# Kernel tuning notes

Measured on AMD Instinct MI355X. Metric: run time of the kernel, lower is better.

## Reference

```python
import jax, jax.numpy as jnp
import numpy as np

N = 100000      # nodes (categories_nums[0])
E = 1600000     # edges
FEAT = 16       # features_num
HID = 32        # hidden
IDE = 16        # id_embed_size
EMB = 8         # embed_size
CAT_MAX = 1000  # categorical vocab (categories_nums[1:])
K = 3           # TAGConv hops (sparse=False)
NC = 2          # num_class
IN_DIM = IDE + 2 * EMB + HID  # 64 -> TAGConv input
EPS = 1e-5


def layer_norm(x, g, b):
    m = jnp.mean(x, axis=-1, keepdims=True)
    v = jnp.mean((x - m) ** 2, axis=-1, keepdims=True)
    return (x - m) * jax.lax.rsqrt(v + EPS) * g + b


def setup_inputs() -> dict:
    key = jax.random.key(0)
    ks = jax.random.split(key, 20)
    s = 0.05
    return {
        "x": jax.random.normal(ks[0], (N, FEAT), jnp.float32),
        "edge_index": jax.random.randint(ks[1], (2, E), 0, N, jnp.int64),
        "edge_weight": jax.random.uniform(ks[2], (E,), jnp.float32),
        "categories_value": jax.random.randint(ks[3], (N, 3), 0, CAT_MAX, jnp.int64),
        "id_table": jax.random.normal(ks[4], (N, IDE), jnp.float32) * s,
        "lin0_id_W": jax.random.normal(ks[5], (IDE, IDE), jnp.float32) * s,
        "lin0_id_b": jnp.zeros((IDE,), jnp.float32),
        "emb1": jax.random.normal(ks[6], (CAT_MAX, EMB), jnp.float32) * s,
        "emb2": jax.random.normal(ks[7], (CAT_MAX, EMB), jnp.float32) * s,
        "lin0_emb_W": jax.random.normal(ks[8], (2 * EMB, 2 * EMB), jnp.float32) * s,
        "lin0_emb_b": jnp.zeros((2 * EMB,), jnp.float32),
        "lin0_W": jax.random.normal(ks[9], (FEAT, HID), jnp.float32) * s,
        "lin0_b": jnp.zeros((HID,), jnp.float32),
        "ln0_g": jnp.ones((IN_DIM,), jnp.float32),
        "ln0_b": jnp.zeros((IN_DIM,), jnp.float32),
        "tag_W": jax.random.normal(ks[10], (K + 1, IN_DIM, HID), jnp.float32) * s,
        "tag_b": jnp.zeros((HID,), jnp.float32),
        "ln1_g": jnp.ones((HID,), jnp.float32),
        "ln1_b": jnp.zeros((HID,), jnp.float32),
        "lin1_W": jax.random.normal(ks[11], (HID, NC), jnp.float32) * s,
        "lin1_b": jnp.zeros((NC,), jnp.float32),
    }


def reference(x, edge_index, edge_weight, categories_value, id_table, lin0_id_W,
              lin0_id_b, emb1, emb2, lin0_emb_W, lin0_emb_b, lin0_W, lin0_b,
              ln0_g, ln0_b, tag_W, tag_b, ln1_g, ln1_b, lin1_W, lin1_b):
    # eval mode: dropouts are identity
    h = jax.nn.elu(x @ lin0_W + lin0_b)                       # [N, HID]
    ide = id_table[categories_value[:, 0]]                    # [N, IDE]
    ide = jax.nn.elu(ide @ lin0_id_W + lin0_id_b)
    er = jnp.concatenate([emb1[categories_value[:, 1]],
                          emb2[categories_value[:, 2]]], axis=1)  # [N, 2*EMB]
    er = jax.nn.elu(er @ lin0_emb_W + lin0_emb_b)
    feat = jnp.concatenate([ide, h, er], axis=1)              # [N, IN_DIM]
    feat = layer_norm(feat, ln0_g, ln0_b)

    # TAGConv: gcn_norm without self-loops, K-hop propagation
    row, col = edge_index[0], edge_index[1]                   # source -> target
    deg = jax.ops.segment_sum(edge_weight, col, num_segments=N)
    dis = jnp.where(deg > 0, deg ** -0.5, 0.0)
    norm = dis[row] * edge_weight * dis[col]                  # [E]

    out = feat @ tag_W[0]                                     # [N, HID]
    xk = feat
    for k in range(1, K + 1):
        xk = jax.ops.segment_sum(xk[row] * norm[:, None], col, num_segments=N)
        out = out + xk @ tag_W[k]
    out = out + tag_b

    out = jax.nn.relu(out)
    out = layer_norm(out, ln1_g, ln1_b)
    out = out @ lin1_W + lin1_b                               # [N, NC]
    return jax.nn.log_softmax(out, axis=-1)
```

## Files before the change

### kernel.cpp

```cpp
#include <hip/hip_runtime.h>
#include <hip/hip_bf16.h>

typedef unsigned short u16;
typedef unsigned int   u32;
typedef unsigned long long u64;
typedef u32 u32x2 __attribute__((ext_vector_type(2)));
typedef u32 u32x4 __attribute__((ext_vector_type(4)));

#define FIX_SCALE 16777216.0f
#define FIX_INV   (1.0f / 16777216.0f)
#define CNT_SHIFT 40
#define DEG_MASK  ((1ULL << CNT_SHIFT) - 1)

__device__ __forceinline__ float b2f(u16 u) { return __uint_as_float(((u32)u) << 16); }
__device__ __forceinline__ u16 f2b(float f) {
    u32 u = __float_as_uint(f);
    return (u16)((u + 0x7FFFu + ((u >> 16) & 1u)) >> 16);
}
__device__ __forceinline__ float elu(float v) { return v > 0.f ? v : expm1f(v); }
__device__ __forceinline__ float ldf(const void* p, size_t i, int f32) {
    return f32 ? ((const float*)p)[i] : b2f(((const u16*)p)[i]);
}
__device__ __forceinline__ float plo(u32 a) { return __uint_as_float(a << 16); }
__device__ __forceinline__ float phi(u32 a) { return __uint_as_float(a & 0xFFFF0000u); }

__global__ void k_flags(const u32* __restrict__ gw, const int* __restrict__ ei,
                        const int* __restrict__ cat, int* __restrict__ flags) {
    if (threadIdx.x == 0 && blockIdx.x == 0) {
        flags[0] = (gw[0] == 0x3F800000u) ? 1 : 0;
        flags[1] = ((ei[1]  | ei[3]  | ei[5]  | ei[7])  == 0) ? 2 : 1;
        flags[2] = ((cat[1] | cat[3] | cat[5] | cat[7]) == 0) ? 2 : 1;
    }
}

__global__ __launch_bounds__(256) void k_feathist(
    const void* __restrict__ x, const int* __restrict__ cat,
    const void* __restrict__ id_table, const void* __restrict__ W_id, const void* __restrict__ b_id,
    const void* __restrict__ emb1, const void* __restrict__ emb2,
    const void* __restrict__ W_emb, const void* __restrict__ b_emb,
    const void* __restrict__ W0, const void* __restrict__ b0,
    const void* __restrict__ g0, const void* __restrict__ bb0,
    u32* __restrict__ feat,
    const int* __restrict__ ei, const void* __restrict__ ew,
    u64* __restrict__ packed, u16* __restrict__ rank,
    const int* __restrict__ flags, int N, int E, int nbN)
{
    __shared__ float sW0[512];
    __shared__ float sb0[32];
    __shared__ float sWid[256];
    __shared__ float sbid[16];
    __shared__ float sWe[256];
    __shared__ float sbe[16];
    __shared__ float sg[64], sb[64];
    int tid = threadIdx.x;
    int f32 = flags[0], s = flags[1], cs = flags[2];

    int e0 = blockIdx.x * 512 + tid;
    int e1 = e0 + 256;
    u64 old0 = 0, old1 = 0;
    bool h0 = (e0 < E), h1 = (e1 < E);
    const int* colp = ei + (size_t)E * s;
    if (h0) {
        int cdst = colp[(size_t)e0 * s];
        float w = ldf(ew, e0, f32);
        old0 = atomicAdd(&packed[cdst], (1ULL << CNT_SHIFT) | (u64)(w * FIX_SCALE + 0.5f));
    }
    if (h1) {
        int cdst = colp[(size_t)e1 * s];
        float w = ldf(ew, e1, f32);
        old1 = atomicAdd(&packed[cdst], (1ULL << CNT_SHIFT) | (u64)(w * FIX_SCALE + 0.5f));
    }

    if (blockIdx.x < nbN) {
        for (int i = tid; i < 512; i += 256) sW0[i] = ldf(W0, i, f32);
        if (tid < 32) sb0[tid] = ldf(b0, tid, f32);
        sWid[tid] = ldf(W_id, tid, f32);
        if (tid < 16) sbid[tid] = ldf(b_id, tid, f32);
        sWe[tid] = ldf(W_emb, tid, f32);
        if (tid < 16) sbe[tid] = ldf(b_emb, tid, f32);
        if (tid < 64) { sg[tid] = ldf(g0, tid, f32); sb[tid] = ldf(bb0, tid, f32); }
        __syncthreads();

        int i = blockIdx.x * 256 + tid;
        if (i < N) {
            size_t cb = (size_t)i * 3 * cs;
            int c0 = cat[cb], c1 = cat[cb + cs], c2 = cat[cb + 2 * cs];
            float f[64];
            {
                float t[16];
                #pragma unroll
                for (int q = 0; q < 16; q++) t[q] = ldf(id_table, (size_t)c0 * 16 + q, f32);
                #pragma unroll
                for (int j = 0; j < 16; j++) {
                    float a = sbid[j];
                    #pragma unroll
                    for (int ff = 0; ff < 16; ff++) a += t[ff] * sWid[ff * 16 + j];
                    f[j] = elu(a);
                }
            }
            {
                float t[16];
                #pragma unroll
                for (int q = 0; q < 16; q++) t[q] = ldf(x, (size_t)i * 16 + q, f32);
                #pragma unroll
                for (int j = 0; j < 32; j++) {
                    float a = sb0[j];
                    #pragma unroll
                    for (int ff = 0; ff < 16; ff++) a += t[ff] * sW0[ff * 32 + j];
                    f[16 + j] = elu(a);
                }
            }
            {
                float t[16];
                #pragma unroll
                for (int q = 0; q < 8; q++) t[q] = ldf(emb1, (size_t)c1 * 8 + q, f32);
                #pragma unroll
                for (int q = 0; q < 8; q++) t[8 + q] = ldf(emb2, (size_t)c2 * 8 + q, f32);
                #pragma unroll
                for (int j = 0; j < 16; j++) {
                    float a = sbe[j];
                    #pragma unroll
                    for (int ff = 0; ff < 16; ff++) a += t[ff] * sWe[ff * 16 + j];
                    f[48 + j] = elu(a);
                }
            }
            float m = 0.f;
            #pragma unroll
            for (int d = 0; d < 64; d++) m += f[d];
            m *= (1.f / 64.f);
            float var = 0.f;
            #pragma unroll
            for (int d = 0; d < 64; d++) { float df = f[d] - m; var += df * df; }
            var *= (1.f / 64.f);
            float rs = rsqrtf(var + 1e-5f);
            #pragma unroll
            for (int d = 0; d < 64; d++) f[d] = (f[d] - m) * rs * sg[d] + sb[d];

            u32* fp = feat + (size_t)i * 32;
            #pragma unroll
            for (int q = 0; q < 32; q++) fp[q] = ((u32)f2b(f[2 * q + 1]) << 16) | f2b(f[2 * q]);
        }
    }
    if (h0) rank[e0] = (u16)(old0 >> CNT_SHIFT);
    if (h1) rank[e1] = (u16)(old1 >> CNT_SHIFT);
}

__global__ __launch_bounds__(256) void k_zproj(
    const u32* __restrict__ feat, const void* __restrict__ tagW,
    float* __restrict__ oacc, u32* __restrict__ z1, u32* __restrict__ z2, u32* __restrict__ z3,
    const int* __restrict__ flags, int N)
{
    __shared__ u32x4 sF[512];
    int tid = threadIdx.x;
    int f32 = flags[0];
    int wid = tid >> 6;
    int lane = tid & 63;
    int j = lane & 31;
    int dh = lane >> 5;

    float w[32];
    {
        size_t base = (size_t)wid * 2048 + (size_t)dh * 1024 + j;
        #pragma unroll
        for (int dd = 0; dd < 32; dd++) w[dd] = ldf(tagW, base + (size_t)dd * 32, f32);
    }

    int nb0 = blockIdx.x * 64;
    int nv = N - nb0; if (nv > 64) nv = 64; if (nv < 0) nv = 0;
    for (int i = tid; i < nv * 8; i += 256)
        sF[i] = ((const u32x4*)feat)[(size_t)nb0 * 8 + i];
    __syncthreads();

    u32* zp = (wid == 1) ? z1 : (wid == 2) ? z2 : z3;

    #pragma unroll 2
    for (int n = 0; n < nv; n++) {
        const u32x4* fp = sF + n * 8 + dh * 4;
        u32x4 r0 = fp[0], r1 = fp[1], r2 = fp[2], r3 = fp[3];
        float za = 0.f, zb = 0.f;
        za += plo(r0.x) * w[0];  zb += phi(r0.x) * w[1];
        za += plo(r0.y) * w[2];  zb += phi(r0.y) * w[3];
        za += plo(r0.z) * w[4];  zb += phi(r0.z) * w[5];
        za += plo(r0.w) * w[6];  zb += phi(r0.w) * w[7];
        za += plo(r1.x) * w[8];  zb += phi(r1.x) * w[9];
        za += plo(r1.y) * w[10]; zb += phi(r1.y) * w[11];
        za += plo(r1.z) * w[12]; zb += phi(r1.z) * w[13];
        za += plo(r1.w) * w[14]; zb += phi(r1.w) * w[15];
        za += plo(r2.x) * w[16]; zb += phi(r2.x) * w[17];
        za += plo(r2.y) * w[18]; zb += phi(r2.y) * w[19];
        za += plo(r2.z) * w[20]; zb += phi(r2.z) * w[21];
        za += plo(r2.w) * w[22]; zb += phi(r2.w) * w[23];
        za += plo(r3.x) * w[24]; zb += phi(r3.x) * w[25];
        za += plo(r3.y) * w[26]; zb += phi(r3.y) * w[27];
        za += plo(r3.z) * w[28]; zb += phi(r3.z) * w[29];
        za += plo(r3.w) * w[30]; zb += phi(r3.w) * w[31];
        float z = za + zb;
        z += __shfl_xor(z, 32);

        int gnode = nb0 + n;
        if (wid == 0) {
            if (lane < 32) oacc[(size_t)gnode * 32 + j] = z;
        } else {
            float zlo = __shfl(z, 2 * lane);
            float zhi = __shfl(z, 2 * lane + 1);
            if (lane < 16)
                zp[(size_t)gnode * 16 + lane] = ((u32)f2b(zhi) << 16) | f2b(zlo);
        }
    }
}

__global__ __launch_bounds__(256) void k_scan1(const u64* __restrict__ packed, int* __restrict__ ebuf,
                                               int* __restrict__ bsum, float* __restrict__ dis, int N)
{
    __shared__ int sdat[256];
    int tid = threadIdx.x;
    int i = blockIdx.x * 256 + tid;
    u64 pv = (i < N) ? packed[i] : 0ULL;
    int v = (int)(pv >> CNT_SHIFT);
    sdat[tid] = v;
    __syncthreads();
    for (int off = 1; off < 256; off <<= 1) {
        int t = (tid >= off) ? sdat[tid - off] : 0;
        __syncthreads();
        sdat[tid] += t;
        __syncthreads();
    }
    if (i < N) {
        ebuf[i] = sdat[tid] - v;
        u64 db = pv & DEG_MASK;
        dis[i] = db ? rsqrtf((float)db * FIX_INV) : 0.f;
    }
    if (tid == 255) bsum[blockIdx.x] = sdat[255];
}

__global__ __launch_bounds__(512) void k_scan2(const int* __restrict__ bsum, int* __restrict__ boff, int NB)
{
    __shared__ int sdat[512];
    __shared__ int scarry;
    int tid = threadIdx.x;
    if (tid == 0) scarry = 0;
    __syncthreads();
    for (int base = 0; base < NB; base += 512) {
        int i = base + tid;
        int v = (i < NB) ? bsum[i] : 0;
        sdat[tid] = v;
        __syncthreads();
        for (int off = 1; off < 512; off <<= 1) {
            int t = (tid >= off) ? sdat[tid - off] : 0;
            __syncthreads();
            sdat[tid] += t;
            __syncthreads();
        }
        if (i < NB) boff[i] = scarry + sdat[tid] - v;
        __syncthreads();
        if (tid == 0) scarry += sdat[511];
        __syncthreads();
    }
}

__global__ __launch_bounds__(256) void k_scan3(const int* __restrict__ ebuf, const int* __restrict__ boff,
                                               int* __restrict__ rowptr, int N, int E)
{
    int i = blockIdx.x * 256 + threadIdx.x;
    if (i >= N) return;
    rowptr[i] = boff[blockIdx.x] + ebuf[i];
    if (i == N - 1) rowptr[N] = E;
}

__global__ __launch_bounds__(256) void k_scatter(const int* __restrict__ ei, const void* __restrict__ ew,
                                                 const float* __restrict__ dis, const u16* __restrict__ rank,
                                                 const int* __restrict__ rowptr, int2* __restrict__ csr,
                                                 const int* __restrict__ flags, int E)
{
    int f32 = flags[0], s = flags[1];
    const int* row = ei;
    const int* col = ei + (size_t)E * s;
    int e = blockIdx.x * 256 + threadIdx.x;
    if (e >= E) return;
    int r = row[(size_t)e * s], c = col[(size_t)e * s];
    float nrm = dis[r] * ldf(ew, e, f32) * dis[c];
    csr[rowptr[c] + (int)rank[e]] = make_int2(r, __float_as_int(nrm));
}

template<int ADD>
__global__ __launch_bounds__(256) void k_ahop(
    const u32* __restrict__ zin, const u32* __restrict__ zadd, u32* __restrict__ uout,
    const int* __restrict__ rowptr, const int2* __restrict__ csr, int N)
{
    int tid = threadIdx.x;
    int node = blockIdx.x * 4 + (tid >> 6);
    if (node >= N) return;
    int lane = tid & 63;
    int o = (lane >> 3) & 7;
    int c = lane & 7;
    int start = rowptr[node], end = rowptr[node + 1];

    const u32x2* fin2 = (const u32x2*)zin;
    float v0 = 0.f, v1 = 0.f, v2 = 0.f, v3 = 0.f;
    int e = start;
    for (; e + 16 <= end; e += 16) {
        int2 ma = csr[e + o];
        int2 mb = csr[e + 8 + o];
        u32x2 aa = fin2[(size_t)(u32)ma.x * 8 + c];
        u32x2 ab = fin2[(size_t)(u32)mb.x * 8 + c];
        float wa = __int_as_float(ma.y), wb = __int_as_float(mb.y);
        v0 += plo(aa.x) * wa; v1 += phi(aa.x) * wa; v2 += plo(aa.y) * wa; v3 += phi(aa.y) * wa;
        v0 += plo(ab.x) * wb; v1 += phi(ab.x) * wb; v2 += plo(ab.y) * wb; v3 += phi(ab.y) * wb;
    }
    for (; e < end; e += 8) {
        int ee = e + o;
        int2 m = (ee < end) ? csr[ee] : make_int2(0, 0);
        u32x2 a = fin2[(size_t)(u32)m.x * 8 + c];
        float w = __int_as_float(m.y);
        v0 += plo(a.x) * w; v1 += phi(a.x) * w; v2 += plo(a.y) * w; v3 += phi(a.y) * w;
    }
    v0 += __shfl_xor(v0, 8);  v1 += __shfl_xor(v1, 8);  v2 += __shfl_xor(v2, 8);  v3 += __shfl_xor(v3, 8);
    v0 += __shfl_xor(v0, 16); v1 += __shfl_xor(v1, 16); v2 += __shfl_xor(v2, 16); v3 += __shfl_xor(v3, 16);
    v0 += __shfl_xor(v0, 32); v1 += __shfl_xor(v1, 32); v2 += __shfl_xor(v2, 32); v3 += __shfl_xor(v3, 32);

    if (lane < 8) {
        if (ADD) {
            u32x2 z = ((const u32x2*)zadd)[(size_t)node * 8 + lane];
            v0 += plo(z.x); v1 += phi(z.x); v2 += plo(z.y); v3 += phi(z.y);
        }
        u32x2 pw;
        pw.x = ((u32)f2b(v1) << 16) | f2b(v0);
        pw.y = ((u32)f2b(v3) << 16) | f2b(v2);
        ((u32x2*)uout)[(size_t)node * 8 + lane] = pw;
    }
}

__global__ __launch_bounds__(256) void k_head(
    const float* __restrict__ oacc, const u32* __restrict__ t1,
    const void* __restrict__ tag_b,
    const void* __restrict__ g1, const void* __restrict__ b1,
    const void* __restrict__ W1, const void* __restrict__ bb1,
    void* __restrict__ out, const int* __restrict__ flags, int N)
{
    __shared__ float stb[32], sg[32], sbb[32], sW1[64], sb1v[2];
    int tid = threadIdx.x;
    int f32 = flags[0];
    if (tid < 32) { stb[tid] = ldf(tag_b, tid, f32); sg[tid] = ldf(g1, tid, f32); sbb[tid] = ldf(b1, tid, f32); }
    if (tid < 64) sW1[tid] = ldf(W1, tid, f32);
    if (tid < 2) sb1v[tid] = ldf(bb1, tid, f32);
    __syncthreads();

    int i = blockIdx.x * 256 + tid;
    if (i >= N) return;

    float acc[32];
    const float4* oa4 = (const float4*)(oacc + (size_t)i * 32);
    #pragma unroll
    for (int q = 0; q < 8; q++) {
        float4 t = oa4[q];
        acc[4 * q] = t.x; acc[4 * q + 1] = t.y; acc[4 * q + 2] = t.z; acc[4 * q + 3] = t.w;
    }
    const u32x2* tp = (const u32x2*)t1 + (size_t)i * 8;
    #pragma unroll
    for (int q = 0; q < 8; q++) {
        u32x2 z = tp[q];
        acc[4 * q]     += plo(z.x); acc[4 * q + 1] += phi(z.x);
        acc[4 * q + 2] += plo(z.y); acc[4 * q + 3] += phi(z.y);
    }
    float o[32]; float m = 0.f;
    #pragma unroll
    for (int j = 0; j < 32; j++) { float t = acc[j] + stb[j]; t = t > 0.f ? t : 0.f; o[j] = t; m += t; }
    m *= (1.f / 32.f);
    float var = 0.f;
    #pragma unroll
    for (int j = 0; j < 32; j++) { float d = o[j] - m; var += d * d; }
    var *= (1.f / 32.f);
    float rs = rsqrtf(var + 1e-5f);
    float z0 = sb1v[0], z1 = sb1v[1];
    #pragma unroll
    for (int j = 0; j < 32; j++) {
        float t = (o[j] - m) * rs * sg[j] + sbb[j];
        z0 += t * sW1[2 * j];
        z1 += t * sW1[2 * j + 1];
    }
    float mx = fmaxf(z0, z1);
    float l = mx + logf(expf(z0 - mx) + expf(z1 - mx));
    if (f32) {
        ((float*)out)[(size_t)i * 2]     = z0 - l;
        ((float*)out)[(size_t)i * 2 + 1] = z1 - l;
    } else {
        *((u32*)((u16*)out + (size_t)i * 2)) = ((u32)f2b(z1 - l) << 16) | f2b(z0 - l);
    }
}

extern "C" void kernel_launch(void* const* d_in, const int* in_sizes, int n_in,
                              void* d_out, int out_size, void* d_ws, size_t ws_size,
                              hipStream_t stream)
{
    const void* x        = d_in[0];
    const int*  ei       = (const int*)d_in[1];
    const void* ew       = d_in[2];
    const int*  cat      = (const int*)d_in[3];
    const void* id_table = d_in[4];
    const void* W_id     = d_in[5];
    const void* b_id     = d_in[6];
    const void* emb1     = d_in[7];
    const void* emb2     = d_in[8];
    const void* W_emb    = d_in[9];
    const void* b_emb    = d_in[10];
    const void* W0       = d_in[11];
    const void* b0       = d_in[12];
    const void* g0       = d_in[13];
    const void* bb0      = d_in[14];
    const void* tagW     = d_in[15];
    const void* tag_b    = d_in[16];
    const void* g1       = d_in[17];
    const void* b1       = d_in[18];
    const void* W1       = d_in[19];
    const void* bb1      = d_in[20];

    int N = in_sizes[0] / 16;
    int E = in_sizes[2];
    int nb = (N + 255) / 256;
    int eb = (E + 255) / 256;
    int eb2 = (E + 511) / 512;
    int zb = (N + 63) / 64;

    char* ws = (char*)d_ws;
    size_t off = 0;
    int*   flags  = (int*)(ws + off);   off += 256;
    float* oacc   = (float*)(ws + off); off += (size_t)N * 32 * 4;
    u32*   feat   = (u32*)(ws + off);   off += (size_t)N * 32 * 4;
    u32*   z1     = (u32*)(ws + off);   off += (size_t)N * 16 * 4;
    u32*   z2     = (u32*)(ws + off);   off += (size_t)N * 16 * 4;
    u32*   z3     = (u32*)(ws + off);   off += (size_t)N * 16 * 4;
    u32*   u2     = (u32*)(ws + off);   off += (size_t)N * 16 * 4;
    int2*  csr    = (int2*)(ws + off);  off += (size_t)E * 8;
    int*   rowptr = (int*)(ws + off);   off += ((size_t)N + 1) * 4;
    off = (off + 255) & ~(size_t)255;
    u16*   rank   = (u16*)(ws + off);   off += (size_t)E * 2;
    off = (off + 255) & ~(size_t)255;
    u64*   packed = (u64*)(ws + off);   off += (size_t)N * 8;
    int*   ebuf   = (int*)(ws + off);   off += (size_t)N * 4;
    float* dis    = (float*)(ws + off); off += (size_t)N * 4;
    int*   bsum   = (int*)(ws + off);   off += (size_t)nb * 4;
    int*   boff   = (int*)(ws + off);   off += (size_t)nb * 4;

    hipMemsetAsync(packed, 0, (size_t)N * 8, stream);
    k_flags<<<1, 64, 0, stream>>>((const u32*)g0, ei, cat, flags);

    k_feathist<<<eb2, 256, 0, stream>>>(x, cat, id_table, W_id, b_id, emb1, emb2, W_emb, b_emb,
                                        W0, b0, g0, bb0, feat,
                                        ei, ew, packed, rank, flags, N, E, nb);
    k_zproj<<<zb, 256, 0, stream>>>(feat, tagW, oacc, z1, z2, z3, flags, N);

    k_scan1<<<nb, 256, 0, stream>>>(packed, ebuf, bsum, dis, N);
    k_scan2<<<1, 512, 0, stream>>>(bsum, boff, nb);
    k_scan3<<<nb, 256, 0, stream>>>(ebuf, boff, rowptr, N, E);
    k_scatter<<<eb, 256, 0, stream>>>(ei, ew, dis, rank, rowptr, csr, flags, E);

    int hb = (N + 3) / 4;
    k_ahop<1><<<hb, 256, 0, stream>>>(z3, z2, u2, rowptr, csr, N);
    k_ahop<1><<<hb, 256, 0, stream>>>(u2, z1, z3, rowptr, csr, N);
    k_ahop<0><<<hb, 256, 0, stream>>>(z3, z1, z2, rowptr, csr, N);
    k_head<<<nb, 256, 0, stream>>>(oacc, z2, tag_b, g1, b1, W1, bb1, d_out, flags, N);
}
```

Before: 386.4 us.

## Fuse output head into final hop and merge block-scan kernels

The final propagation hop now runs the bias, ReLU, LayerNorm, linear layer and log-softmax itself, using 8-lane shuffles across the per-node lanes. This removes the separate head kernel and the write and re-read of the last hop result. The second and third scan kernels are also merged into one: each block recomputes its offset by summing all preceding block sums. That drops a single-block launch but adds redundant reads of the block sums, which grow with the block index.

```diff
diff --git a/kernel.cpp b/kernel.cpp
--- a/kernel.cpp
+++ b/kernel.cpp
@@ -233,37 +233,23 @@
     if (tid == 255) bsum[blockIdx.x] = sdat[255];
 }
 
-__global__ __launch_bounds__(512) void k_scan2(const int* __restrict__ bsum, int* __restrict__ boff, int NB)
-{
-    __shared__ int sdat[512];
-    __shared__ int scarry;
+__global__ __launch_bounds__(256) void k_scanX(const int* __restrict__ bsum, const int* __restrict__ ebuf,
+                                               int* __restrict__ rowptr, int N, int E)
+{
+    __shared__ int sred[256];
+    int b = blockIdx.x;
     int tid = threadIdx.x;
-    if (tid == 0) scarry = 0;
+    int acc = 0;
+    for (int i = tid; i < b; i += 256) acc += bsum[i];
+    sred[tid] = acc;
     __syncthreads();
-    for (int base = 0; base < NB; base += 512) {
-        int i = base + tid;
-        int v = (i < NB) ? bsum[i] : 0;
-        sdat[tid] = v;
+    for (int off = 128; off > 0; off >>= 1) {
+        if (tid < off) sred[tid] += sred[tid + off];
         __syncthreads();
-        for (int off = 1; off < 512; off <<= 1) {
-            int t = (tid >= off) ? sdat[tid - off] : 0;
-            __syncthreads();
-            sdat[tid] += t;
-            __syncthreads();
-        }
-        if (i < NB) boff[i] = scarry + sdat[tid] - v;
-        __syncthreads();
-        if (tid == 0) scarry += sdat[511];
-        __syncthreads();
-    }
-}
-
-__global__ __launch_bounds__(256) void k_scan3(const int* __restrict__ ebuf, const int* __restrict__ boff,
-                                               int* __restrict__ rowptr, int N, int E)
-{
-    int i = blockIdx.x * 256 + threadIdx.x;
-    if (i >= N) return;
-    rowptr[i] = boff[blockIdx.x] + ebuf[i];
+    }
+    int boffb = sred[0];
+    int i = b * 256 + tid;
+    if (i < N) rowptr[i] = boffb + ebuf[i];
     if (i == N - 1) rowptr[N] = E;
 }
 
@@ -282,10 +268,14 @@
     csr[rowptr[c] + (int)rank[e]] = make_int2(r, __float_as_int(nrm));
 }
 
-template<int ADD>
+template<int ADD, int HEAD>
 __global__ __launch_bounds__(256) void k_ahop(
     const u32* __restrict__ zin, const u32* __restrict__ zadd, u32* __restrict__ uout,
-    const int* __restrict__ rowptr, const int2* __restrict__ csr, int N)
+    const int* __restrict__ rowptr, const int2* __restrict__ csr,
+    const float* __restrict__ oacc, const void* __restrict__ tag_b,
+    const void* __restrict__ g1, const void* __restrict__ b1,
+    const void* __restrict__ W1, const void* __restrict__ bb1,
+    void* __restrict__ out, const int* __restrict__ flags, int N)
 {
     int tid = threadIdx.x;
     int node = blockIdx.x * 4 + (tid >> 6);
@@ -318,73 +308,57 @@
     v0 += __shfl_xor(v0, 16); v1 += __shfl_xor(v1, 16); v2 += __shfl_xor(v2, 16); v3 += __shfl_xor(v3, 16);
     v0 += __shfl_xor(v0, 32); v1 += __shfl_xor(v1, 32); v2 += __shfl_xor(v2, 32); v3 += __shfl_xor(v3, 32);
 
-    if (lane < 8) {
-        if (ADD) {
-            u32x2 z = ((const u32x2*)zadd)[(size_t)node * 8 + lane];
-            v0 += plo(z.x); v1 += phi(z.x); v2 += plo(z.y); v3 += phi(z.y);
+    if (!HEAD) {
+        if (lane < 8) {
+            if (ADD) {
+                u32x2 z = ((const u32x2*)zadd)[(size_t)node * 8 + lane];
+                v0 += plo(z.x); v1 += phi(z.x); v2 += plo(z.y); v3 += phi(z.y);
+            }
+            u32x2 pw;
+            pw.x = ((u32)f2b(v1) << 16) | f2b(v0);
+            pw.y = ((u32)f2b(v3) << 16) | f2b(v2);
+            ((u32x2*)uout)[(size_t)node * 8 + lane] = pw;
         }
-        u32x2 pw;
-        pw.x = ((u32)f2b(v1) << 16) | f2b(v0);
-        pw.y = ((u32)f2b(v3) << 16) | f2b(v2);
-        ((u32x2*)uout)[(size_t)node * 8 + lane] = pw;
-    }
-}
-
-__global__ __launch_bounds__(256) void k_head(
-    const float* __restrict__ oacc, const u32* __restrict__ t1,
-    const void* __restrict__ tag_b,
-    const void* __restrict__ g1, const void* __restrict__ b1,
-    const void* __restrict__ W1, const void* __restrict__ bb1,
-    void* __restrict__ out, const int* __restrict__ flags, int N)
-{
-    __shared__ float stb[32], sg[32], sbb[32], sW1[64], sb1v[2];
-    int tid = threadIdx.x;
-    int f32 = flags[0];
-    if (tid < 32) { stb[tid] = ldf(tag_b, tid, f32); sg[tid] = ldf(g1, tid, f32); sbb[tid] = ldf(b1, tid, f32); }
-    if (tid < 64) sW1[tid] = ldf(W1, tid, f32);
-    if (tid < 2) sb1v[tid] = ldf(bb1, tid, f32);
-    __syncthreads();
-
-    int i = blockIdx.x * 256 + tid;
-    if (i >= N) return;
-
-    float acc[32];
-    const float4* oa4 = (const float4*)(oacc + (size_t)i * 32);
-    #pragma unroll
-    for (int q = 0; q < 8; q++) {
-        float4 t = oa4[q];
-        acc[4 * q] = t.x; acc[4 * q + 1] = t.y; acc[4 * q + 2] = t.z; acc[4 * q + 3] = t.w;
-    }
-    const u32x2* tp = (const u32x2*)t1 + (size_t)i * 8;
-    #pragma unroll
-    for (int q = 0; q < 8; q++) {
-        u32x2 z = tp[q];
-        acc[4 * q]     += plo(z.x); acc[4 * q + 1] += phi(z.x);
-        acc[4 * q + 2] += plo(z.y); acc[4 * q + 3] += phi(z.y);
-    }
-    float o[32]; float m = 0.f;
-    #pragma unroll
-    for (int j = 0; j < 32; j++) { float t = acc[j] + stb[j]; t = t > 0.f ? t : 0.f; o[j] = t; m += t; }
-    m *= (1.f / 32.f);
-    float var = 0.f;
-    #pragma unroll
-    for (int j = 0; j < 32; j++) { float d = o[j] - m; var += d * d; }
-    var *= (1.f / 32.f);
-    float rs = rsqrtf(var + 1e-5f);
-    float z0 = sb1v[0], z1 = sb1v[1];
-    #pragma unroll
-    for (int j = 0; j < 32; j++) {
-        float t = (o[j] - m) * rs * sg[j] + sbb[j];
-        z0 += t * sW1[2 * j];
-        z1 += t * sW1[2 * j + 1];
-    }
-    float mx = fmaxf(z0, z1);
-    float l = mx + logf(expf(z0 - mx) + expf(z1 - mx));
-    if (f32) {
-        ((float*)out)[(size_t)i * 2]     = z0 - l;
-        ((float*)out)[(size_t)i * 2 + 1] = z1 - l;
     } else {
-        *((u32*)((u16*)out + (size_t)i * 2)) = ((u32)f2b(z1 - l) << 16) | f2b(z0 - l);
+        int f32 = flags[0];
+        float4 oa = ((const float4*)(oacc + (size_t)node * 32))[c];
+        float t0 = oa.x + v0 + ldf(tag_b, 4 * c + 0, f32);
+        float t1v = oa.y + v1 + ldf(tag_b, 4 * c + 1, f32);
+        float t2 = oa.z + v2 + ldf(tag_b, 4 * c + 2, f32);
+        float t3 = oa.w + v3 + ldf(tag_b, 4 * c + 3, f32);
+        t0 = t0 > 0.f ? t0 : 0.f;
+        t1v = t1v > 0.f ? t1v : 0.f;
+        t2 = t2 > 0.f ? t2 : 0.f;
+        t3 = t3 > 0.f ? t3 : 0.f;
+        float sm = t0 + t1v + t2 + t3;
+        sm += __shfl_xor(sm, 1); sm += __shfl_xor(sm, 2); sm += __shfl_xor(sm, 4);
+        float m = sm * (1.f / 32.f);
+        float d0 = t0 - m, d1 = t1v - m, d2 = t2 - m, d3 = t3 - m;
+        float vq = d0 * d0 + d1 * d1 + d2 * d2 + d3 * d3;
+        vq += __shfl_xor(vq, 1); vq += __shfl_xor(vq, 2); vq += __shfl_xor(vq, 4);
+        float rs = rsqrtf(vq * (1.f / 32.f) + 1e-5f);
+        float y0 = d0 * rs * ldf(g1, 4 * c + 0, f32) + ldf(b1, 4 * c + 0, f32);
+        float y1 = d1 * rs * ldf(g1, 4 * c + 1, f32) + ldf(b1, 4 * c + 1, f32);
+        float y2 = d2 * rs * ldf(g1, 4 * c + 2, f32) + ldf(b1, 4 * c + 2, f32);
+        float y3 = d3 * rs * ldf(g1, 4 * c + 3, f32) + ldf(b1, 4 * c + 3, f32);
+        float z0 = y0 * ldf(W1, 8 * c + 0, f32) + y1 * ldf(W1, 8 * c + 2, f32)
+                 + y2 * ldf(W1, 8 * c + 4, f32) + y3 * ldf(W1, 8 * c + 6, f32);
+        float z1 = y0 * ldf(W1, 8 * c + 1, f32) + y1 * ldf(W1, 8 * c + 3, f32)
+                 + y2 * ldf(W1, 8 * c + 5, f32) + y3 * ldf(W1, 8 * c + 7, f32);
+        z0 += __shfl_xor(z0, 1); z0 += __shfl_xor(z0, 2); z0 += __shfl_xor(z0, 4);
+        z1 += __shfl_xor(z1, 1); z1 += __shfl_xor(z1, 2); z1 += __shfl_xor(z1, 4);
+        if (lane == 0) {
+            z0 += ldf(bb1, 0, f32);
+            z1 += ldf(bb1, 1, f32);
+            float mx = fmaxf(z0, z1);
+            float l = mx + logf(expf(z0 - mx) + expf(z1 - mx));
+            if (f32) {
+                ((float*)out)[(size_t)node * 2]     = z0 - l;
+                ((float*)out)[(size_t)node * 2 + 1] = z1 - l;
+            } else {
+                *((u32*)((u16*)out + (size_t)node * 2)) = ((u32)f2b(z1 - l) << 16) | f2b(z0 - l);
+            }
+        }
     }
 }
 
@@ -439,7 +413,6 @@
     int*   ebuf   = (int*)(ws + off);   off += (size_t)N * 4;
     float* dis    = (float*)(ws + off); off += (size_t)N * 4;
     int*   bsum   = (int*)(ws + off);   off += (size_t)nb * 4;
-    int*   boff   = (int*)(ws + off);   off += (size_t)nb * 4;
 
     hipMemsetAsync(packed, 0, (size_t)N * 8, stream);
     k_flags<<<1, 64, 0, stream>>>((const u32*)g0, ei, cat, flags);
@@ -450,13 +423,17 @@
     k_zproj<<<zb, 256, 0, stream>>>(feat, tagW, oacc, z1, z2, z3, flags, N);
 
     k_scan1<<<nb, 256, 0, stream>>>(packed, ebuf, bsum, dis, N);
-    k_scan2<<<1, 512, 0, stream>>>(bsum, boff, nb);
-    k_scan3<<<nb, 256, 0, stream>>>(ebuf, boff, rowptr, N, E);
+    k_scanX<<<nb, 256, 0, stream>>>(bsum, ebuf, rowptr, N, E);
     k_scatter<<<eb, 256, 0, stream>>>(ei, ew, dis, rank, rowptr, csr, flags, E);
 
     int hb = (N + 3) / 4;
-    k_ahop<1><<<hb, 256, 0, stream>>>(z3, z2, u2, rowptr, csr, N);
-    k_ahop<1><<<hb, 256, 0, stream>>>(u2, z1, z3, rowptr, csr, N);
-    k_ahop<0><<<hb, 256, 0, stream>>>(z3, z1, z2, rowptr, csr, N);
-    k_head<<<nb, 256, 0, stream>>>(oacc, z2, tag_b, g1, b1, W1, bb1, d_out, flags, N);
-}
+    k_ahop<1, 0><<<hb, 256, 0, stream>>>(z3, z2, u2, rowptr, csr,
+                                         nullptr, nullptr, nullptr, nullptr, nullptr, nullptr,
+                                         nullptr, flags, N);
+    k_ahop<1, 0><<<hb, 256, 0, stream>>>(u2, z1, z3, rowptr, csr,
+                                         nullptr, nullptr, nullptr, nullptr, nullptr, nullptr,
+                                         nullptr, flags, N);
+    k_ahop<0, 1><<<hb, 256, 0, stream>>>(z3, nullptr, nullptr, rowptr, csr,
+                                         oacc, tag_b, g1, b1, W1, bb1,
+                                         d_out, flags, N);
+}
```

Result: slower. 457.1 us (+18.3%).
